# Performance work log

Measured on AMD Instinct MI355X. Metric: run time of the kernel, lower is better.

Reference implementation:

```python
import jax, jax.numpy as jnp
import numpy as np

N, D = 16384, 2048

def setup_inputs() -> dict:
    key = jax.random.key(0)
    k1, k2 = jax.random.split(key)
    cxr = jax.random.normal(k1, (N, D), dtype=jnp.float32)
    ehr = jax.random.normal(k2, (N, D), dtype=jnp.float32)
    return {"cxr": cxr, "ehr": ehr}

def reference(cxr, ehr):
    # Same math as diag(a_norm @ b_norm.T): row-wise cosine similarity.
    # a_norm = ehr / ||ehr||_row, b_norm = cxr / ||cxr||_row (L2 norms, dim=1)
    a_norm = ehr / jnp.linalg.norm(ehr, axis=1, keepdims=True)
    b_norm = cxr / jnp.linalg.norm(cxr, axis=1, keepdims=True)
    cos = jnp.sum(a_norm * b_norm, axis=1)  # [N] row-wise dot products
    return 1.0 - jnp.mean(cos)
```

## Files before the change

### kernel.cpp

```cpp
#include <hip/hip_runtime.h>
#include <hip/hip_bf16.h>


#define ROWS 16384
#define COLS_V4 512
#define BLOCK 512
#define GRID 512
#define STEPS (ROWS / GRID)
#define WPB (BLOCK / 64)

__global__ __launch_bounds__(BLOCK, 2) void cosine_partial_kernel(
    const float4* __restrict__ A,
    const float4* __restrict__ B,
    float* __restrict__ partial) {
    const int t    = threadIdx.x;
    const int wave = t >> 6;
    const int lane = t & 63;

    __shared__ float s_part[STEPS][WPB][3];

    const float4* __restrict__ a = A + (size_t)blockIdx.x * COLS_V4 + t;
    const float4* __restrict__ b = B + (size_t)blockIdx.x * COLS_V4 + t;
    const size_t stride = (size_t)GRID * COLS_V4;

    float4 x = a[0];
    float4 y = b[0];
    for (int s = 0; s < STEPS; ++s) {
        float4 xn, yn;
        if (s + 1 < STEPS) {
            xn = a[(size_t)(s + 1) * stride];
            yn = b[(size_t)(s + 1) * stride];
        }
        float d  = x.x * y.x + x.y * y.y + x.z * y.z + x.w * y.w;
        float na = x.x * x.x + x.y * x.y + x.z * x.z + x.w * x.w;
        float nb = y.x * y.x + y.y * y.y + y.z * y.z + y.w * y.w;
        #pragma unroll
        for (int off = 32; off > 0; off >>= 1) {
            d  += __shfl_down(d,  off, 64);
            na += __shfl_down(na, off, 64);
            nb += __shfl_down(nb, off, 64);
        }
        if (lane == 0) {
            s_part[s][wave][0] = d;
            s_part[s][wave][1] = na;
            s_part[s][wave][2] = nb;
        }
        x = xn;
        y = yn;
    }
    __syncthreads();

    float loss = 0.f;
    if (t < STEPS) {
        float d = 0.f, na = 0.f, nb = 0.f;
        #pragma unroll
        for (int w = 0; w < WPB; ++w) {
            d  += s_part[t][w][0];
            na += s_part[t][w][1];
            nb += s_part[t][w][2];
        }
        loss = 1.0f - d * rsqrtf(na * nb);
    }
    if (wave == 0) {
        #pragma unroll
        for (int off = 16; off > 0; off >>= 1)
            loss += __shfl_down(loss, off, 64);
        if (lane == 0) partial[blockIdx.x] = loss;
    }
}

__global__ __launch_bounds__(256) void cosine_reduce_kernel(
    const float* __restrict__ partial,
    float* __restrict__ out) {
    const int t = threadIdx.x;
    float s = partial[t] + partial[t + 256];
    #pragma unroll
    for (int off = 32; off > 0; off >>= 1) s += __shfl_down(s, off, 64);

    __shared__ float s_sum[4];
    const int wave = t >> 6;
    const int lane = t & 63;
    if (lane == 0) s_sum[wave] = s;
    __syncthreads();
    if (t == 0) {
        out[0] = (s_sum[0] + s_sum[1] + s_sum[2] + s_sum[3]) * (1.0f / (float)ROWS);
    }
}

extern "C" void kernel_launch(void* const* d_in, const int* in_sizes, int n_in,
                              void* d_out, int out_size, void* d_ws, size_t ws_size,
                              hipStream_t stream) {
    const float4* cxr = (const float4*)d_in[0];
    const float4* ehr = (const float4*)d_in[1];
    float* out     = (float*)d_out;
    float* partial = (float*)d_ws;

    cosine_partial_kernel<<<GRID, BLOCK, 0, stream>>>(cxr, ehr, partial);
    cosine_reduce_kernel<<<1, 256, 0, stream>>>(partial, out);
}
```

Before: 272.8 us.

## Assign whole rows to each wavefront with 16 outstanding float4 loads per lane

Measured after the change: 274.6 us. About the same (+0.7%).

```diff
diff --git a/kernel.cpp b/kernel.cpp
--- a/kernel.cpp
+++ b/kernel.cpp
@@ -1,71 +1,63 @@
 #include <hip/hip_runtime.h>
-#include <hip/hip_bf16.h>
 
 
 #define ROWS 16384
 #define COLS_V4 512
-#define BLOCK 512
-#define GRID 512
-#define STEPS (ROWS / GRID)
+#define BLOCK 256
 #define WPB (BLOCK / 64)
+#define GRID 1024
+#define RPW (ROWS / (GRID * WPB))
 
-__global__ __launch_bounds__(BLOCK, 2) void cosine_partial_kernel(
+__global__ __launch_bounds__(BLOCK, 4) void cosine_partial_kernel(
     const float4* __restrict__ A,
     const float4* __restrict__ B,
     float* __restrict__ partial) {
     const int t    = threadIdx.x;
     const int wave = t >> 6;
     const int lane = t & 63;
+    const int row0 = (blockIdx.x * WPB + wave) * RPW;
 
-    __shared__ float s_part[STEPS][WPB][3];
+    float wloss = 0.0f;
 
-    const float4* __restrict__ a = A + (size_t)blockIdx.x * COLS_V4 + t;
-    const float4* __restrict__ b = B + (size_t)blockIdx.x * COLS_V4 + t;
-    const size_t stride = (size_t)GRID * COLS_V4;
+    for (int r = 0; r < RPW; ++r) {
+        const size_t base = (size_t)(row0 + r) * COLS_V4 + lane;
+        const float4* __restrict__ a = A + base;
+        const float4* __restrict__ b = B + base;
 
-    float4 x = a[0];
-    float4 y = b[0];
-    for (int s = 0; s < STEPS; ++s) {
-        float4 xn, yn;
-        if (s + 1 < STEPS) {
-            xn = a[(size_t)(s + 1) * stride];
-            yn = b[(size_t)(s + 1) * stride];
+        float4 va[8], vb[8];
+        #pragma unroll
+        for (int c = 0; c < 8; ++c) va[c] = a[(size_t)c * 64];
+        #pragma unroll
+        for (int c = 0; c < 8; ++c) vb[c] = b[(size_t)c * 64];
+
+        float d = 0.0f, na = 0.0f, nb = 0.0f;
+        #pragma unroll
+        for (int c = 0; c < 8; ++c) {
+            d  += va[c].x * vb[c].x + va[c].y * vb[c].y
+                + va[c].z * vb[c].z + va[c].w * vb[c].w;
+            na += va[c].x * va[c].x + va[c].y * va[c].y
+                + va[c].z * va[c].z + va[c].w * va[c].w;
+            nb += vb[c].x * vb[c].x + vb[c].y * vb[c].y
+                + vb[c].z * vb[c].z + vb[c].w * vb[c].w;
         }
-        float d  = x.x * y.x + x.y * y.y + x.z * y.z + x.w * y.w;
-        float na = x.x * x.x + x.y * x.y + x.z * x.z + x.w * x.w;
-        float nb = y.x * y.x + y.y * y.y + y.z * y.z + y.w * y.w;
+
         #pragma unroll
         for (int off = 32; off > 0; off >>= 1) {
             d  += __shfl_down(d,  off, 64);
             na += __shfl_down(na, off, 64);
             nb += __shfl_down(nb, off, 64);
         }
-        if (lane == 0) {
-            s_part[s][wave][0] = d;
-            s_part[s][wave][1] = na;
-            s_part[s][wave][2] = nb;
-        }
-        x = xn;
-        y = yn;
+        if (lane == 0) wloss += 1.0f - d * rsqrtf(na * nb);
     }
+
+    __shared__ float s_loss[WPB];
+    if (lane == 0) s_loss[wave] = wloss;
     __syncthreads();
-
-    float loss = 0.f;
-    if (t < STEPS) {
-        float d = 0.f, na = 0.f, nb = 0.f;
+    if (t == 0) {
+        float s = 0.0f;
         #pragma unroll
-        for (int w = 0; w < WPB; ++w) {
-            d  += s_part[t][w][0];
-            na += s_part[t][w][1];
-            nb += s_part[t][w][2];
-        }
-        loss = 1.0f - d * rsqrtf(na * nb);
-    }
-    if (wave == 0) {
-        #pragma unroll
-        for (int off = 16; off > 0; off >>= 1)
-            loss += __shfl_down(loss, off, 64);
-        if (lane == 0) partial[blockIdx.x] = loss;
+        for (int w = 0; w < WPB; ++w) s += s_loss[w];
+        partial[blockIdx.x] = s;
     }
 }
 
@@ -73,7 +65,7 @@
     const float* __restrict__ partial,
     float* __restrict__ out) {
     const int t = threadIdx.x;
-    float s = partial[t] + partial[t + 256];
+    float s = partial[t] + partial[t + 256] + partial[t + 512] + partial[t + 768];
     #pragma unroll
     for (int off = 32; off > 0; off >>= 1) s += __shfl_down(s, off, 64);
 
```

## Stage rows through LDS with async global_load_lds triple-buffer pipeline

Applied to the files above, without the earlier changes.

Measured after the change: 256.0 us. 1.07x faster.

```diff
diff --git a/kernel.cpp b/kernel.cpp
--- a/kernel.cpp
+++ b/kernel.cpp
@@ -1,39 +1,61 @@
 #include <hip/hip_runtime.h>
-#include <hip/hip_bf16.h>
 
 
 #define ROWS 16384
-#define COLS_V4 512
+#define COLS 2048
 #define BLOCK 512
 #define GRID 512
 #define STEPS (ROWS / GRID)
 #define WPB (BLOCK / 64)
+#define PIPE 3
 
-__global__ __launch_bounds__(BLOCK, 2) void cosine_partial_kernel(
-    const float4* __restrict__ A,
-    const float4* __restrict__ B,
+typedef float v4f __attribute__((ext_vector_type(4)));
+
+__device__ __forceinline__ void stage_row(
+    const float* __restrict__ g, v4f* lds_slice_base) {
+    __builtin_amdgcn_global_load_lds(
+        (const __attribute__((address_space(1))) void*)g,
+        (__attribute__((address_space(3))) void*)lds_slice_base,
+        16, 0, 2);
+}
+
+__global__ __launch_bounds__(BLOCK, 4) void cosine_partial_kernel(
+    const float* __restrict__ A,
+    const float* __restrict__ B,
     float* __restrict__ partial) {
     const int t    = threadIdx.x;
     const int wave = t >> 6;
     const int lane = t & 63;
+    const int row0 = blockIdx.x * STEPS;
 
+    __shared__ v4f bufA[PIPE][BLOCK];
+    __shared__ v4f bufB[PIPE][BLOCK];
     __shared__ float s_part[STEPS][WPB][3];
 
-    const float4* __restrict__ a = A + (size_t)blockIdx.x * COLS_V4 + t;
-    const float4* __restrict__ b = B + (size_t)blockIdx.x * COLS_V4 + t;
-    const size_t stride = (size_t)GRID * COLS_V4;
+    #pragma unroll
+    for (int s = 0; s < PIPE; ++s) {
+        const size_t gbase = (size_t)(row0 + s) * COLS + (size_t)t * 4;
+        stage_row(A + gbase, &bufA[s][wave * 64]);
+        stage_row(B + gbase, &bufB[s][wave * 64]);
+    }
 
-    float4 x = a[0];
-    float4 y = b[0];
+    int p = 0;
     for (int s = 0; s < STEPS; ++s) {
-        float4 xn, yn;
-        if (s + 1 < STEPS) {
-            xn = a[(size_t)(s + 1) * stride];
-            yn = b[(size_t)(s + 1) * stride];
+        if (s <= STEPS - 3) {
+            asm volatile("s_waitcnt vmcnt(4)" ::: "memory");
+        } else if (s == STEPS - 2) {
+            asm volatile("s_waitcnt vmcnt(2)" ::: "memory");
+        } else {
+            asm volatile("s_waitcnt vmcnt(0)" ::: "memory");
         }
-        float d  = x.x * y.x + x.y * y.y + x.z * y.z + x.w * y.w;
-        float na = x.x * x.x + x.y * x.y + x.z * x.z + x.w * x.w;
-        float nb = y.x * y.x + y.y * y.y + y.z * y.z + y.w * y.w;
+        __builtin_amdgcn_sched_barrier(0);
+
+        v4f va = bufA[p][t];
+        v4f vb = bufB[p][t];
+        float d  = va.x * vb.x + va.y * vb.y + va.z * vb.z + va.w * vb.w;
+        float na = va.x * va.x + va.y * va.y + va.z * va.z + va.w * va.w;
+        float nb = vb.x * vb.x + vb.y * vb.y + vb.z * vb.z + vb.w * vb.w;
+
         #pragma unroll
         for (int off = 32; off > 0; off >>= 1) {
             d  += __shfl_down(d,  off, 64);
@@ -45,9 +67,16 @@
             s_part[s][wave][1] = na;
             s_part[s][wave][2] = nb;
         }
-        x = xn;
-        y = yn;
+
+        __builtin_amdgcn_sched_barrier(0);
+        if (s + PIPE < STEPS) {
+            const size_t gbase = (size_t)(row0 + s + PIPE) * COLS + (size_t)t * 4;
+            stage_row(A + gbase, &bufA[p][wave * 64]);
+            stage_row(B + gbase, &bufB[p][wave * 64]);
+        }
+        if (++p == PIPE) p = 0;
     }
+
     __syncthreads();
 
     float loss = 0.f;
@@ -90,8 +119,8 @@
 extern "C" void kernel_launch(void* const* d_in, const int* in_sizes, int n_in,
                               void* d_out, int out_size, void* d_ws, size_t ws_size,
                               hipStream_t stream) {
-    const float4* cxr = (const float4*)d_in[0];
-    const float4* ehr = (const float4*)d_in[1];
+    const float* cxr = (const float*)d_in[0];
+    const float* ehr = (const float*)d_in[1];
     float* out     = (float*)d_out;
     float* partial = (float*)d_ws;
 
```
